# Kernel tuning notes

Measured on AMD Instinct MI355X. Metric: run time of the kernel, lower is better.

Reference implementation:

```python
import jax, jax.numpy as jnp
import numpy as np

N = 50000; FIN = 64; H = 128; E = 800000; T = 8
P = 250000; D = 500000; G = 20000; V = 2000; O = 2


def _mp(h, Ws, Wn, b, edge_src, edge_dst, n):
    # mean-aggregation message passing: relu(h Ws + mean_neigh(h) Wn + b)
    deg = jax.ops.segment_sum(jnp.ones(edge_dst.shape[0], h.dtype), edge_dst, n)
    agg = jax.ops.segment_sum(h[edge_src], edge_dst, n) / jnp.maximum(deg, 1.0)[:, None]
    return jax.nn.relu(h @ Ws + agg @ Wn + b)


def _forward(x, W_enc_self, W_enc_nei, b_enc, W2_self, W2_nei, b2, Wd1, bd1, Wd2, bd2,
             counts, edge_src, edge_dst, place_idx, src_idx, t_idx, dst_nodes, dst_seg,
             group_id, variant_of_group):
    n = x.shape[0]
    p = place_idx.shape[0]
    g = variant_of_group.shape[0]
    v = counts.shape[0]
    # first encoder, then T sequential second_encoder applications (feature generations)
    h0 = _mp(x, W_enc_self, W_enc_nei, b_enc, edge_src, edge_dst, n)

    def step(h, _):
        h2 = _mp(h, W2_self, W2_nei, b2, edge_src, edge_dst, n)
        return h2, h2

    _, hs = jax.lax.scan(step, h0, None, length=T)
    feats = jnp.concatenate([h0[None], hs], axis=0)  # [T+1, N, H]

    # gather (place, src) features at the generation index of each prediction
    place_f = feats[t_idx, place_idx]                 # [P, H]
    src_f = feats[t_idx, src_idx]                     # [P, H]
    # dst feature = sum over the destination set of each prediction
    dst_f = jax.ops.segment_sum(feats[t_idx[dst_seg], dst_nodes], dst_seg, p)  # [P, H]

    cat = jnp.concatenate([place_f, src_f, dst_f], axis=-1)  # [P, 3H]
    logits = jax.nn.relu(cat @ Wd1 + bd1) @ Wd2 + bd2        # [P, O]
    logprob = jax.nn.log_softmax(logits, axis=-1)            # [P, O]

    # prev_prob: inclusive running sum of per-step logprob sums within each variant
    group_sums = jax.ops.segment_sum(logprob, group_id, g)   # [G, O]
    cum = jnp.cumsum(group_sums, axis=0)
    var_tot = jax.ops.segment_sum(group_sums, variant_of_group, v)
    var_excl = jnp.cumsum(var_tot, axis=0) - var_tot
    within = cum - var_excl[variant_of_group]                # [G, O]
    prev = within[group_id]                                  # [P, O]

    logc = jnp.log(counts / jnp.sum(counts))                 # log(count/total) per variant
    add = logprob + prev + logc[variant_of_group[group_id]][:, None]
    return jnp.zeros((n, logits.shape[-1]), x.dtype).at[place_idx].add(add)


def setup_inputs() -> dict:
    ks = jax.random.split(jax.random.key(0), 24)
    s = jnp.float32(0.05)
    f32 = jnp.float32
    i32 = jnp.int32
    return {
        "x": jax.random.normal(ks[0], (N, FIN), f32),
        "W_enc_self": jax.random.normal(ks[1], (FIN, H), f32) * s,
        "W_enc_nei": jax.random.normal(ks[2], (FIN, H), f32) * s,
        "b_enc": jax.random.normal(ks[3], (H,), f32) * s,
        "W2_self": jax.random.normal(ks[4], (H, H), f32) * s,
        "W2_nei": jax.random.normal(ks[5], (H, H), f32) * s,
        "b2": jax.random.normal(ks[6], (H,), f32) * s,
        "Wd1": jax.random.normal(ks[7], (3 * H, 3 * H), f32) * s,
        "bd1": jax.random.normal(ks[8], (3 * H,), f32) * s,
        "Wd2": jax.random.normal(ks[9], (3 * H, O), f32) * s,
        "bd2": jax.random.normal(ks[10], (O,), f32) * s,
        "counts": jax.random.uniform(ks[11], (V,), f32) + 0.5,
        "edge_src": jax.random.randint(ks[12], (E,), 0, N, i32),
        "edge_dst": jax.random.randint(ks[13], (E,), 0, N, i32),
        "place_idx": jax.random.randint(ks[14], (P,), 0, N, i32),
        "src_idx": jax.random.randint(ks[15], (P,), 0, N, i32),
        "t_idx": jax.random.randint(ks[16], (P,), 0, T + 1, i32),
        "dst_nodes": jax.random.randint(ks[17], (D,), 0, N, i32),
        "dst_seg": jnp.sort(jax.random.randint(ks[18], (D,), 0, P, i32)),
        "group_id": jnp.sort(jax.random.randint(ks[19], (P,), 0, G, i32)),
        "variant_of_group": jnp.sort(jax.random.randint(ks[20], (G,), 0, V, i32)),
    }


def reference(x, W_enc_self, W_enc_nei, b_enc, W2_self, W2_nei, b2, Wd1, bd1, Wd2, bd2,
              counts, edge_src, edge_dst, place_idx, src_idx, t_idx, dst_nodes, dst_seg,
              group_id, variant_of_group):
    return _forward(x, W_enc_self, W_enc_nei, b_enc, W2_self, W2_nei, b2, Wd1, bd1, Wd2, bd2,
                    counts, edge_src, edge_dst, place_idx, src_idx, t_idx, dst_nodes, dst_seg,
                    group_id, variant_of_group)
```

## Files before the change

kernel.cpp:

```cpp
#include <hip/hip_runtime.h>
#include <math.h>

#define NN 50000
#define FINN 64
#define HD 128
#define EE 800000
#define TT 8
#define PP 250000
#define DD 500000
#define GG 20000
#define VV 2000
#define OO 2

typedef short short8 __attribute__((ext_vector_type(8)));
typedef float f32x4 __attribute__((ext_vector_type(4)));

__device__ __forceinline__ unsigned short f2bf(float f) {
    unsigned int u = __float_as_uint(f);
    u += 0x7fffu + ((u >> 16) & 1u);
    return (unsigned short)(u >> 16);
}
__device__ __forceinline__ float bf2f(unsigned short u) {
    return __uint_as_float(((unsigned int)u) << 16);
}

struct us8 { unsigned short v[8]; };

__device__ __forceinline__ void gload_lds16(const void* g, void* l) {
    __builtin_amdgcn_global_load_lds((__attribute__((address_space(1))) void*)g,
                                     (__attribute__((address_space(3))) void*)l, 16, 0, 0);
}

__global__ void count_k(const int* __restrict__ idx, int* __restrict__ counts, int n) {
    int i = blockIdx.x * blockDim.x + threadIdx.x;
    if (i < n) atomicAdd(&counts[idx[i]], 1);
}

__global__ void blk_sum_k(const int* __restrict__ counts, int n, int* __restrict__ bsum) {
    __shared__ int buf[256];
    int t = threadIdx.x, i = blockIdx.x * 256 + t;
    buf[t] = (i < n) ? counts[i] : 0;
    __syncthreads();
    for (int off = 128; off > 0; off >>= 1) {
        if (t < off) buf[t] += buf[t + off];
        __syncthreads();
    }
    if (t == 0) bsum[blockIdx.x] = buf[0];
}

__global__ void scan_small_k(const int* __restrict__ bsum, int nb, int* __restrict__ boff) {
    __shared__ int buf[256];
    int t = threadIdx.x;
    int v = (t < nb) ? bsum[t] : 0;
    buf[t] = v;
    __syncthreads();
    for (int off = 1; off < 256; off <<= 1) {
        int u = (t >= off) ? buf[t - off] : 0;
        __syncthreads();
        buf[t] += u;
        __syncthreads();
    }
    if (t < nb) boff[t] = buf[t] - v;
}

__global__ void rowptr_fill_k(const int* __restrict__ counts, const int* __restrict__ boff,
                              int n, int* __restrict__ rowptr, int total) {
    __shared__ int buf[256];
    int t = threadIdx.x, i = blockIdx.x * 256 + t;
    int v = (i < n) ? counts[i] : 0;
    buf[t] = v;
    __syncthreads();
    for (int off = 1; off < 256; off <<= 1) {
        int u = (t >= off) ? buf[t - off] : 0;
        __syncthreads();
        buf[t] += u;
        __syncthreads();
    }
    if (i < n) rowptr[i] = boff[blockIdx.x] + buf[t] - v;
    if (i == 0) rowptr[n] = total;
}

__global__ void lb_rowptr_k(const int* __restrict__ arr, int n, int* __restrict__ rowptr, int m) {
    int i = blockIdx.x * blockDim.x + threadIdx.x;
    if (i > m) return;
    int lo = 0, hi = n;
    while (lo < hi) {
        int mid = (lo + hi) >> 1;
        if (arr[mid] < i) lo = mid + 1; else hi = mid;
    }
    rowptr[i] = lo;
}

__global__ void fill_csr_k(const int* __restrict__ esrc, const int* __restrict__ edst,
                           const int* __restrict__ rowptr, int* __restrict__ cursor,
                           int* __restrict__ outi, int n) {
    int e = blockIdx.x * blockDim.x + threadIdx.x;
    if (e < n) {
        int d = edst[e];
        int pos = atomicAdd(&cursor[d], 1);
        outi[rowptr[d] + pos] = esrc[e];
    }
}

__global__ void hist9_k(const int* __restrict__ t_idx, int* __restrict__ hist) {
    __shared__ int l[9];
    if (threadIdx.x < 9) l[threadIdx.x] = 0;
    __syncthreads();
    int p = blockIdx.x * 256 + threadIdx.x;
    if (p < PP) atomicAdd(&l[t_idx[p]], 1);
    __syncthreads();
    if (threadIdx.x < 9) atomicAdd(&hist[threadIdx.x], l[threadIdx.x]);
}

__global__ void scan9_k(const int* __restrict__ hist, int* __restrict__ boff9) {
    if (threadIdx.x == 0) {
        int a = 0;
        for (int i = 0; i < 9; ++i) { boff9[i] = a; a += hist[i]; }
    }
}

__global__ void bucket_perm_k(const int* __restrict__ t_idx, const int* __restrict__ boff9,
                              int* __restrict__ cursor9, int* __restrict__ pperm) {
    __shared__ int lcnt[9];
    __shared__ int lbase[9];
    int tid = threadIdx.x;
    int p = blockIdx.x * 256 + tid;
    if (tid < 9) lcnt[tid] = 0;
    __syncthreads();
    int t = 0, lr = 0;
    bool ok = p < PP;
    if (ok) {
        t = t_idx[p];
        lr = atomicAdd(&lcnt[t], 1);
    }
    __syncthreads();
    if (tid < 9) lbase[tid] = atomicAdd(&cursor9[tid], lcnt[tid]);
    __syncthreads();
    if (ok) pperm[boff9[t] + lbase[t] + lr] = p;
}

__global__ void prep_k(const float* __restrict__ x,
                       const float* __restrict__ Wes, const float* __restrict__ Wen,
                       const float* __restrict__ W2s, const float* __restrict__ W2n,
                       const float* __restrict__ Wd1,
                       unsigned short* __restrict__ xb, unsigned short* __restrict__ wenc_t,
                       unsigned short* __restrict__ w2_t, unsigned short* __restrict__ wd1t) {
    int i = blockIdx.x * 256 + threadIdx.x;
    if (i < NN * FINN) xb[i] = f2bf(x[i]);
    if (i < HD * 2 * FINN) {
        int c = i / (2 * FINN), k = i - c * (2 * FINN);
        wenc_t[i] = f2bf((k < FINN) ? Wes[k * HD + c] : Wen[(k - FINN) * HD + c]);
    }
    if (i < HD * 2 * HD) {
        int c = i / (2 * HD), k = i - c * (2 * HD);
        w2_t[i] = f2bf((k < HD) ? W2s[k * HD + c] : W2n[(k - HD) * HD + c]);
    }
    if (i < 384 * 384) {
        int n = i / 384, k = i - n * 384;
        wd1t[i] = f2bf(Wd1[k * 384 + n]);
    }
}

template <int KIN>
__launch_bounds__(256)
__global__ void agg2_k(const unsigned short* __restrict__ h, const int* __restrict__ rowptr,
                       const int* __restrict__ csr_src, unsigned short* __restrict__ aggout) {
    constexpr int LPR = KIN >> 3;
    constexpr int EPW = 64 / LPR;
    int node = blockIdx.x * 4 + (threadIdx.x >> 6);
    int lane = threadIdx.x & 63;
    int sub = lane / LPR;
    int fl = lane % LPR;
    if (node >= NN) return;
    int s = rowptr[node], e = rowptr[node + 1];
    float acc[8] = {};
    int i = s + sub;
    int iB = i + EPW;
    int srcA = (i < e) ? csr_src[i] : 0;
    int srcB = (iB < e) ? csr_src[iB] : 0;
    while (i < e) {
        bool hB = iB < e;
        us8 vA = *(const us8*)&h[(size_t)srcA * KIN + fl * 8];
        us8 vB;
        if (hB) vB = *(const us8*)&h[(size_t)srcB * KIN + fl * 8];
        int iN = iB + EPW, iN2 = iN + EPW;
        srcA = (iN < e) ? csr_src[iN] : 0;
        srcB = (iN2 < e) ? csr_src[iN2] : 0;
#pragma unroll
        for (int j = 0; j < 8; ++j) acc[j] += bf2f(vA.v[j]);
        if (hB) {
#pragma unroll
            for (int j = 0; j < 8; ++j) acc[j] += bf2f(vB.v[j]);
        }
        i = iN; iB = iN2;
    }
#pragma unroll
    for (int m = LPR; m < 64; m <<= 1)
#pragma unroll
        for (int j = 0; j < 8; ++j) acc[j] += __shfl_xor(acc[j], m);
    if (sub == 0) {
        float d = fmaxf((float)(e - s), 1.f);
        us8 o;
#pragma unroll
        for (int j = 0; j < 8; ++j) o.v[j] = f2bf(acc[j] / d);
        *(us8*)&aggout[(size_t)node * KIN + fl * 8] = o;
    }
}

__launch_bounds__(128)
__global__ void mp_mfma_k(const unsigned short* __restrict__ hin,
                          const unsigned short* __restrict__ aggin,
                          const unsigned short* __restrict__ Wt,
                          const float* __restrict__ bias,
                          unsigned short* __restrict__ hout, int Kin) {
    int tid = threadIdx.x;
    int lane = tid & 63, w = tid >> 6;
    int cc = lane & 15, g = lane >> 4;
    int K = 2 * Kin;
    int rowA = blockIdx.x * 32 + w * 16 + cc;
    bool rowok = rowA < NN;
    const unsigned short* hrow = hin + (size_t)rowA * Kin;
    const unsigned short* arow = aggin + (size_t)rowA * Kin;

    f32x4 acc[8];
#pragma unroll
    for (int t = 0; t < 8; ++t) acc[t] = (f32x4){0.f, 0.f, 0.f, 0.f};

    for (int k0 = 0; k0 < K; k0 += 32) {
        int k = k0 + g * 8;
        short8 a = {0, 0, 0, 0, 0, 0, 0, 0};
        if (rowok)
            a = *(const short8*)((k < Kin) ? (hrow + k) : (arow + (k - Kin)));
#pragma unroll
        for (int t = 0; t < 8; ++t) {
            short8 b = *(const short8*)&Wt[(size_t)(t * 16 + cc) * K + k];
            acc[t] = __builtin_amdgcn_mfma_f32_16x16x32_bf16(a, b, acc[t], 0, 0, 0);
        }
    }
#pragma unroll
    for (int t = 0; t < 8; ++t) {
        int col = t * 16 + cc;
        float b1 = bias[col];
#pragma unroll
        for (int r = 0; r < 4; ++r) {
            int grow = blockIdx.x * 32 + w * 16 + g * 4 + r;
            if (grow < NN)
                hout[(size_t)grow * HD + col] = f2bf(fmaxf(acc[t][r] + b1, 0.f));
        }
    }
}

__launch_bounds__(256)
__global__ void dst_sum_k(const unsigned short* __restrict__ feats,
                          const int* __restrict__ t_idx, const int* __restrict__ dst_nodes,
                          const int* __restrict__ dst_rowptr, const int* __restrict__ pperm,
                          unsigned short* __restrict__ dstc) {
    int pi = blockIdx.x * 4 + (threadIdx.x >> 6);
    int lane = threadIdx.x & 63;
    int sub = lane >> 4;
    int fl = lane & 15;
    if (pi >= PP) return;
    int p = pperm[pi];
    long t = t_idx[p];
    const unsigned short* base = feats + t * (long)NN * HD;
    int s = dst_rowptr[p], e = dst_rowptr[p + 1];
    float acc[8] = {};
    int i = s + sub;
    int nd_next = (i < e) ? dst_nodes[i] : 0;
    for (; i < e; i += 4) {
        int nd = nd_next;
        int in = i + 4;
        if (in < e) nd_next = dst_nodes[in];
        us8 v = *(const us8*)&base[(size_t)nd * HD + fl * 8];
#pragma unroll
        for (int j = 0; j < 8; ++j) acc[j] += bf2f(v.v[j]);
    }
#pragma unroll
    for (int m = 16; m < 64; m <<= 1)
#pragma unroll
        for (int j = 0; j < 8; ++j) acc[j] += __shfl_xor(acc[j], m);
    if (sub == 0) {
        us8 o;
#pragma unroll
        for (int j = 0; j < 8; ++j) o.v[j] = f2bf(acc[j]);
        *(us8*)&dstc[(size_t)pi * HD + fl * 8] = o;
    }
}

__launch_bounds__(256)
__global__ void dec3_k(const unsigned short* __restrict__ feats,
                       const unsigned short* __restrict__ dstc,
                       const int* __restrict__ place_idx, const int* __restrict__ src_idx,
                       const int* __restrict__ t_idx, const int* __restrict__ group_id,
                       const int* __restrict__ pperm,
                       const unsigned short* __restrict__ Wd1t,
                       const float* __restrict__ bd1, const float* __restrict__ Wd2,
                       const float* __restrict__ bd2, float* __restrict__ logprob,
                       float* __restrict__ group_sums) {
    __shared__ unsigned short lds_a[192 * 128];
    __shared__ const unsigned short* rowbase[192];
    __shared__ float lpart[4][64][2];

    int tid = threadIdx.x;
    int lane = tid & 63, w = tid >> 6;
    int cc = lane & 15, gq = lane >> 4;
    int p0 = blockIdx.x * 64;

    if (tid < 192) {
        int sec = tid >> 6, pl = tid & 63;
        int pic = min(p0 + pl, PP - 1);
        const unsigned short* b;
        if (sec == 2) {
            b = dstc + (size_t)pic * HD;
        } else {
            int p = pperm[pic];
            long t = t_idx[p];
            int node = (sec == 0) ? place_idx[p] : src_idx[p];
            b = feats + ((t * NN + node) * (long)HD);
        }
        rowbase[tid] = b;
    }
    __syncthreads();

    {
        int chunk = lane & 15;
        int rsub = lane >> 4;
#pragma unroll
        for (int i = 0; i < 12; ++i) {
            int r = w * 48 + i * 4 + rsub;
            const unsigned short* src = rowbase[r] + ((chunk ^ (r & 7)) * 8);
            gload_lds16(src, &lds_a[(size_t)(w * 48 + i * 4) * 128]);
        }
    }
    __syncthreads();

    f32x4 acc[4][6];
#pragma unroll
    for (int s = 0; s < 4; ++s)
#pragma unroll
        for (int t = 0; t < 6; ++t) acc[s][t] = (f32x4){0.f, 0.f, 0.f, 0.f};

    const unsigned short* bbase = Wd1t + ((long)(w * 96 + cc) * 384 + gq * 8);
    int cx7 = cc & 7;

#pragma unroll
    for (int kk = 0; kk < 12; ++kk) {
        int sec = kk >> 2;
        int cbase = (kk & 3) * 4 + gq;
        int coff = (cbase ^ cx7) * 8;
        short8 a_c[4];
#pragma unroll
        for (int s = 0; s < 4; ++s) {
            int lrow = sec * 64 + s * 16 + cc;
            a_c[s] = *(const short8*)&lds_a[(size_t)lrow * 128 + coff];
        }
#pragma unroll
        for (int t = 0; t < 6; ++t) {
            short8 b = *(const short8*)(bbase + (long)t * 16 * 384 + kk * 32);
#pragma unroll
            for (int s = 0; s < 4; ++s)
                acc[s][t] = __builtin_amdgcn_mfma_f32_16x16x32_bf16(a_c[s], b, acc[s][t], 0, 0, 0);
        }
    }

    float part[4][4][2] = {};
#pragma unroll
    for (int t = 0; t < 6; ++t) {
        int col = w * 96 + t * 16 + cc;
        float b1 = bd1[col];
        float w0 = Wd2[col * 2 + 0], w1 = Wd2[col * 2 + 1];
#pragma unroll
        for (int s = 0; s < 4; ++s)
#pragma unroll
            for (int r = 0; r < 4; ++r) {
                float h = fmaxf(acc[s][t][r] + b1, 0.f);
                part[s][r][0] += h * w0;
                part[s][r][1] += h * w1;
            }
    }
#pragma unroll
    for (int m = 1; m < 16; m <<= 1)
#pragma unroll
        for (int s = 0; s < 4; ++s)
#pragma unroll
            for (int r = 0; r < 4; ++r) {
                part[s][r][0] += __shfl_xor(part[s][r][0], m);
                part[s][r][1] += __shfl_xor(part[s][r][1], m);
            }
    if (cc == 0) {
#pragma unroll
        for (int s = 0; s < 4; ++s)
#pragma unroll
            for (int r = 0; r < 4; ++r) {
                int row = s * 16 + gq * 4 + r;
                lpart[w][row][0] = part[s][r][0];
                lpart[w][row][1] = part[s][r][1];
            }
    }
    __syncthreads();
    if (tid < 64) {
        int pi = p0 + tid;
        if (pi < PP) {
            int p = pperm[pi];
            float l0 = lpart[0][tid][0] + lpart[1][tid][0] + lpart[2][tid][0] + lpart[3][tid][0] + bd2[0];
            float l1 = lpart[0][tid][1] + lpart[1][tid][1] + lpart[2][tid][1] + lpart[3][tid][1] + bd2[1];
            float m = fmaxf(l0, l1);
            float lse = m + logf(expf(l0 - m) + expf(l1 - m));
            float lp0 = l0 - lse, lp1 = l1 - lse;
            logprob[p * 2 + 0] = lp0;
            logprob[p * 2 + 1] = lp1;
            int g = group_id[p];
            atomicAdd(&group_sums[g * 2 + 0], lp0);
            atomicAdd(&group_sums[g * 2 + 1], lp1);
        }
    }
}

__global__ void within_total_k(const float* __restrict__ group_sums,
                               const int* __restrict__ var_rowptr,
                               const float* __restrict__ counts,
                               float* __restrict__ within, float* __restrict__ total) {
    __shared__ float buf[256];
    int tid = threadIdx.x;
    float s = 0.f;
    for (int i = tid; i < VV; i += 256) s += counts[i];
    buf[tid] = s;
    __syncthreads();
    for (int off = 128; off > 0; off >>= 1) {
        if (tid < off) buf[tid] += buf[tid + off];
        __syncthreads();
    }
    if (tid == 0) total[0] = buf[0];
    for (int v = tid; v < VV; v += 256) {
        int gs = var_rowptr[v], ge = var_rowptr[v + 1];
        float r0 = 0.f, r1 = 0.f;
        for (int g = gs; g < ge; ++g) {
            r0 += group_sums[2 * g + 0];
            r1 += group_sums[2 * g + 1];
            within[2 * g + 0] = r0;
            within[2 * g + 1] = r1;
        }
    }
}

__global__ void final_k(const float* __restrict__ logprob, const float* __restrict__ within,
                        const int* __restrict__ group_id, const int* __restrict__ vog,
                        const float* __restrict__ counts, const float* __restrict__ total,
                        const int* __restrict__ place_idx, float* __restrict__ outp) {
    int p = blockIdx.x * blockDim.x + threadIdx.x;
    if (p >= PP) return;
    int g = group_id[p];
    int v = vog[g];
    float lc = logf(counts[v]) - logf(total[0]);
    int node = place_idx[p];
    atomicAdd(&outp[node * 2 + 0], logprob[p * 2 + 0] + within[g * 2 + 0] + lc);
    atomicAdd(&outp[node * 2 + 1], logprob[p * 2 + 1] + within[g * 2 + 1] + lc);
}

extern "C" void kernel_launch(void* const* d_in, const int* in_sizes, int n_in,
                              void* d_out, int out_size, void* d_ws, size_t ws_size,
                              hipStream_t stream) {
    const float* x          = (const float*)d_in[0];
    const float* W_enc_self = (const float*)d_in[1];
    const float* W_enc_nei  = (const float*)d_in[2];
    const float* b_enc      = (const float*)d_in[3];
    const float* W2_self    = (const float*)d_in[4];
    const float* W2_nei     = (const float*)d_in[5];
    const float* b2         = (const float*)d_in[6];
    const float* Wd1        = (const float*)d_in[7];
    const float* bd1        = (const float*)d_in[8];
    const float* Wd2        = (const float*)d_in[9];
    const float* bd2        = (const float*)d_in[10];
    const float* counts     = (const float*)d_in[11];
    const int* edge_src     = (const int*)d_in[12];
    const int* edge_dst     = (const int*)d_in[13];
    const int* place_idx    = (const int*)d_in[14];
    const int* src_idx      = (const int*)d_in[15];
    const int* t_idx        = (const int*)d_in[16];
    const int* dst_nodes    = (const int*)d_in[17];
    const int* dst_seg      = (const int*)d_in[18];
    const int* group_id     = (const int*)d_in[19];
    const int* variant_of_group = (const int*)d_in[20];
    float* outp = (float*)d_out;

    const int NB = (NN + 255) / 256;

    unsigned short* feats = (unsigned short*)d_ws;
    unsigned short* aggb  = feats + (size_t)(TT + 1) * NN * HD;
    unsigned short* xb    = aggb + (size_t)NN * HD;
    unsigned short* dstc  = xb + (size_t)NN * FINN;
    unsigned short* wenc_t = dstc + (size_t)PP * HD;
    unsigned short* w2_t   = wenc_t + HD * 2 * FINN;
    unsigned short* wd1t   = w2_t + HD * 2 * HD;
    int* zr = (int*)(wd1t + 384 * 384);
    int* csr_counts   = zr;
    int* csr_cursor   = csr_counts + NN;
    float* group_sums = (float*)(csr_cursor + NN);
    int* hist9        = (int*)(group_sums + 2 * GG);
    int* cursor9      = hist9 + 9;
    size_t zero_words = (size_t)NN + NN + 2 * GG + 18;
    int* bsum       = cursor9 + 9;
    int* boff       = bsum + 256;
    int* boff9      = boff + 256;
    int* csr_rowptr = boff9 + 16;
    int* dst_rowptr = csr_rowptr + (NN + 1);
    int* var_rowptr = dst_rowptr + (PP + 1);
    int* csr_src    = var_rowptr + (VV + 1);
    int* pperm      = csr_src + EE;
    float* logprob  = (float*)(pperm + PP);
    float* within   = logprob + 2 * PP;
    float* total_counts = within + 2 * GG;

    hipMemsetAsync(zr, 0, zero_words * 4, stream);
    hipMemsetAsync(d_out, 0, (size_t)out_size * sizeof(float), stream);

    prep_k<<<(NN * FINN + 255) / 256, 256, 0, stream>>>(x, W_enc_self, W_enc_nei, W2_self,
                                                        W2_nei, Wd1, xb, wenc_t, w2_t, wd1t);
    count_k<<<(EE + 255) / 256, 256, 0, stream>>>(edge_dst, csr_counts, EE);
    blk_sum_k<<<NB, 256, 0, stream>>>(csr_counts, NN, bsum);
    scan_small_k<<<1, 256, 0, stream>>>(bsum, NB, boff);
    rowptr_fill_k<<<NB, 256, 0, stream>>>(csr_counts, boff, NN, csr_rowptr, EE);
    fill_csr_k<<<(EE + 255) / 256, 256, 0, stream>>>(edge_src, edge_dst, csr_rowptr,
                                                     csr_cursor, csr_src, EE);
    lb_rowptr_k<<<(PP + 256) / 256, 256, 0, stream>>>(dst_seg, DD, dst_rowptr, PP);
    lb_rowptr_k<<<(VV + 256) / 256, 256, 0, stream>>>(variant_of_group, GG, var_rowptr, VV);
    hist9_k<<<(PP + 255) / 256, 256, 0, stream>>>(t_idx, hist9);
    scan9_k<<<1, 64, 0, stream>>>(hist9, boff9);
    bucket_perm_k<<<(PP + 255) / 256, 256, 0, stream>>>(t_idx, boff9, cursor9, pperm);

    for (int r = 0; r <= TT; ++r) {
        const unsigned short* hin = (r == 0) ? xb : feats + (size_t)(r - 1) * NN * HD;
        unsigned short* hout = feats + (size_t)r * NN * HD;
        if (r == 0) {
            agg2_k<FINN><<<(NN + 3) / 4, 256, 0, stream>>>(hin, csr_rowptr, csr_src, aggb);
            mp_mfma_k<<<(NN + 31) / 32, 128, 0, stream>>>(hin, aggb, wenc_t, b_enc, hout, FINN);
        } else {
            agg2_k<HD><<<(NN + 3) / 4, 256, 0, stream>>>(hin, csr_rowptr, csr_src, aggb);
            mp_mfma_k<<<(NN + 31) / 32, 128, 0, stream>>>(hin, aggb, w2_t, b2, hout, HD);
        }
    }

    dst_sum_k<<<(PP + 3) / 4, 256, 0, stream>>>(feats, t_idx, dst_nodes, dst_rowptr, pperm, dstc);
    dec3_k<<<(PP + 63) / 64, 256, 0, stream>>>(feats, dstc, place_idx, src_idx, t_idx,
                                               group_id, pperm, wd1t, bd1, Wd2, bd2,
                                               logprob, group_sums);

    within_total_k<<<1, 256, 0, stream>>>(group_sums, var_rowptr, counts, within, total_counts);
    final_k<<<(PP + 255) / 256, 256, 0, stream>>>(logprob, within, group_id, variant_of_group,
                                                  counts, total_counts, place_idx, outp);
}
```

Measured before the change: 1.132 ms.

## Make decoder kernel persistent with double-buffered LDS gathers and register-resident weights

The decoder kernel becomes persistent: a fixed grid of 256 blocks loops over the row tiles. Each block keeps its whole Wd1 slice in registers instead of reloading it for every tile. Row gathers into LDS are double-buffered and their index and pointer lookups are prefetched several tiles ahead, so global-to-LDS loads overlap the MFMA work of the previous tile. The cost is heavy register pressure (72 short8 values per thread, launch bounds of 1) and hand-written waitcnt and barrier handling that could be fragile.

```diff
diff --git a/kernel.cpp b/kernel.cpp
--- a/kernel.cpp
+++ b/kernel.cpp
@@ -11,6 +11,9 @@
 #define GG 20000
 #define VV 2000
 #define OO 2
+
+#define DEC_GRID 256
+#define DEC_TILES ((PP + 63) / 64)
 
 typedef short short8 __attribute__((ext_vector_type(8)));
 typedef float f32x4 __attribute__((ext_vector_type(4)));
@@ -287,8 +290,8 @@
     }
 }
 
-__launch_bounds__(256)
-__global__ void dec3_k(const unsigned short* __restrict__ feats,
+__launch_bounds__(256, 1)
+__global__ void dec4_k(const unsigned short* __restrict__ feats,
                        const unsigned short* __restrict__ dstc,
                        const int* __restrict__ place_idx, const int* __restrict__ src_idx,
                        const int* __restrict__ t_idx, const int* __restrict__ group_id,
@@ -297,123 +300,170 @@
                        const float* __restrict__ bd1, const float* __restrict__ Wd2,
                        const float* __restrict__ bd2, float* __restrict__ logprob,
                        float* __restrict__ group_sums) {
-    __shared__ unsigned short lds_a[192 * 128];
-    __shared__ const unsigned short* rowbase[192];
+    __shared__ unsigned short buf[2][192 * 128];
+    __shared__ unsigned long long rb[2][192];
     __shared__ float lpart[4][64][2];
 
     int tid = threadIdx.x;
     int lane = tid & 63, w = tid >> 6;
     int cc = lane & 15, gq = lane >> 4;
-    int p0 = blockIdx.x * 64;
-
+    int cx7 = cc & 7;
+    int bid = blockIdx.x;
+
+    int row = min(tid, 191);
+    int sec = row >> 6, pl = row & 63;
+    const int* nptr = (sec == 0) ? place_idx : src_idx;
+
+    int nt = (DEC_TILES - 1 - bid) / DEC_GRID + 1;
+
+    int pic0 = min(bid * 64 + pl, PP - 1);
+    int pic1 = min((bid + DEC_GRID) * 64 + pl, PP - 1);
+    int pic2p = min((bid + 2 * DEC_GRID) * 64 + pl, PP - 1);
+    int pA = pperm[pic0], pB = pperm[pic1];
+    int preg = pperm[pic2p];
+    int tA = t_idx[pA], tB = t_idx[pB];
+    int nA = nptr[pA], nB = nptr[pB];
     if (tid < 192) {
-        int sec = tid >> 6, pl = tid & 63;
-        int pic = min(p0 + pl, PP - 1);
-        const unsigned short* b;
-        if (sec == 2) {
-            b = dstc + (size_t)pic * HD;
-        } else {
-            int p = pperm[pic];
-            long t = t_idx[p];
-            int node = (sec == 0) ? place_idx[p] : src_idx[p];
-            b = feats + ((t * NN + node) * (long)HD);
-        }
-        rowbase[tid] = b;
-    }
-    __syncthreads();
-
+        rb[0][tid] = (sec == 2) ? (unsigned long long)(dstc + (size_t)pic0 * HD)
+                                : (unsigned long long)(feats + (((long)tA * NN + nA) * (long)HD));
+        rb[1][tid] = (sec == 2) ? (unsigned long long)(dstc + (size_t)pic1 * HD)
+                                : (unsigned long long)(feats + (((long)tB * NN + nB) * (long)HD));
+    }
+
+    short8 breg[72];
     {
-        int chunk = lane & 15;
-        int rsub = lane >> 4;
-#pragma unroll
-        for (int i = 0; i < 12; ++i) {
-            int r = w * 48 + i * 4 + rsub;
-            const unsigned short* src = rowbase[r] + ((chunk ^ (r & 7)) * 8);
-            gload_lds16(src, &lds_a[(size_t)(w * 48 + i * 4) * 128]);
-        }
-    }
-    __syncthreads();
-
-    f32x4 acc[4][6];
-#pragma unroll
-    for (int s = 0; s < 4; ++s)
-#pragma unroll
-        for (int t = 0; t < 6; ++t) acc[s][t] = (f32x4){0.f, 0.f, 0.f, 0.f};
-
-    const unsigned short* bbase = Wd1t + ((long)(w * 96 + cc) * 384 + gq * 8);
-    int cx7 = cc & 7;
-
-#pragma unroll
-    for (int kk = 0; kk < 12; ++kk) {
-        int sec = kk >> 2;
-        int cbase = (kk & 3) * 4 + gq;
-        int coff = (cbase ^ cx7) * 8;
-        short8 a_c[4];
-#pragma unroll
-        for (int s = 0; s < 4; ++s) {
-            int lrow = sec * 64 + s * 16 + cc;
-            a_c[s] = *(const short8*)&lds_a[(size_t)lrow * 128 + coff];
-        }
+        const unsigned short* bbase = Wd1t + ((long)(w * 96 + cc) * 384 + gq * 8);
+#pragma unroll
+        for (int kk = 0; kk < 12; ++kk)
+#pragma unroll
+            for (int t = 0; t < 6; ++t)
+                breg[kk * 6 + t] = *(const short8*)(bbase + (long)t * 16 * 384 + kk * 32);
+    }
+    __syncthreads();
+
+    int rsub = lane >> 4, chunk = lane & 15;
+
+#define STAGE(par_)                                                                  \
+    {                                                                                \
+        _Pragma("unroll")                                                            \
+        for (int i = 0; i < 12; ++i) {                                               \
+            int r = w * 48 + i * 4 + rsub;                                           \
+            const unsigned short* src =                                              \
+                (const unsigned short*)rb[par_][r] + ((chunk ^ (r & 7)) * 8);        \
+            gload_lds16(src, &buf[par_][(w * 48 + i * 4) * 128]);                    \
+        }                                                                            \
+    }
+
+    STAGE(0);
+
+    for (int k = 0; k < nt; ++k) {
+        int par = k & 1, npar = par ^ 1;
+        int tl = bid + k * DEC_GRID;
+
+        int tload = t_idx[preg];
+        int nload = nptr[preg];
+        int pic3v = min((bid + (k + 3) * DEC_GRID) * 64 + pl, PP - 1);
+        int preg2 = pperm[pic3v];
+        int pic2v = min((bid + (k + 2) * DEC_GRID) * 64 + pl, PP - 1);
+
+        STAGE(npar);
+
+        __builtin_amdgcn_sched_barrier(0);
+        asm volatile("s_waitcnt vmcnt(15)" ::: "memory");
+        __builtin_amdgcn_s_barrier();
+        __builtin_amdgcn_sched_barrier(0);
+
+        const unsigned short* bufc = &buf[par][0];
+        f32x4 acc[4][6];
+#pragma unroll
+        for (int s = 0; s < 4; ++s)
+#pragma unroll
+            for (int t = 0; t < 6; ++t) acc[s][t] = (f32x4){0.f, 0.f, 0.f, 0.f};
+
+#pragma unroll
+        for (int kk = 0; kk < 12; ++kk) {
+            int seck = kk >> 2;
+            int cbase = (kk & 3) * 4 + gq;
+            int coff = (cbase ^ cx7) * 8;
+            short8 a_c[4];
+#pragma unroll
+            for (int s = 0; s < 4; ++s) {
+                int lrow = seck * 64 + s * 16 + cc;
+                a_c[s] = *(const short8*)&bufc[lrow * 128 + coff];
+            }
+#pragma unroll
+            for (int t = 0; t < 6; ++t)
+#pragma unroll
+                for (int s = 0; s < 4; ++s)
+                    acc[s][t] = __builtin_amdgcn_mfma_f32_16x16x32_bf16(a_c[s], breg[kk * 6 + t],
+                                                                        acc[s][t], 0, 0, 0);
+        }
+
+        float part[4][4][2] = {};
 #pragma unroll
         for (int t = 0; t < 6; ++t) {
-            short8 b = *(const short8*)(bbase + (long)t * 16 * 384 + kk * 32);
+            int col = w * 96 + t * 16 + cc;
+            float b1 = bd1[col];
+            float w0 = Wd2[col * 2 + 0], w1 = Wd2[col * 2 + 1];
 #pragma unroll
             for (int s = 0; s < 4; ++s)
-                acc[s][t] = __builtin_amdgcn_mfma_f32_16x16x32_bf16(a_c[s], b, acc[s][t], 0, 0, 0);
-        }
-    }
-
-    float part[4][4][2] = {};
-#pragma unroll
-    for (int t = 0; t < 6; ++t) {
-        int col = w * 96 + t * 16 + cc;
-        float b1 = bd1[col];
-        float w0 = Wd2[col * 2 + 0], w1 = Wd2[col * 2 + 1];
-#pragma unroll
-        for (int s = 0; s < 4; ++s)
-#pragma unroll
-            for (int r = 0; r < 4; ++r) {
-                float h = fmaxf(acc[s][t][r] + b1, 0.f);
-                part[s][r][0] += h * w0;
-                part[s][r][1] += h * w1;
+#pragma unroll
+                for (int r = 0; r < 4; ++r) {
+                    float h = fmaxf(acc[s][t][r] + b1, 0.f);
+                    part[s][r][0] += h * w0;
+                    part[s][r][1] += h * w1;
+                }
+        }
+#pragma unroll
+        for (int m = 1; m < 16; m <<= 1)
+#pragma unroll
+            for (int s = 0; s < 4; ++s)
+#pragma unroll
+                for (int r = 0; r < 4; ++r) {
+                    part[s][r][0] += __shfl_xor(part[s][r][0], m);
+                    part[s][r][1] += __shfl_xor(part[s][r][1], m);
+                }
+        if (cc == 0) {
+#pragma unroll
+            for (int s = 0; s < 4; ++s)
+#pragma unroll
+                for (int r = 0; r < 4; ++r) {
+                    int orow = s * 16 + gq * 4 + r;
+                    lpart[w][orow][0] = part[s][r][0];
+                    lpart[w][orow][1] = part[s][r][1];
+                }
+        }
+
+        if (tid < 192)
+            rb[par][tid] = (sec == 2)
+                               ? (unsigned long long)(dstc + (size_t)pic2v * HD)
+                               : (unsigned long long)(feats + (((long)tload * NN + nload) * (long)HD));
+        preg = preg2;
+
+        asm volatile("s_waitcnt lgkmcnt(0)" ::: "memory");
+        __builtin_amdgcn_s_barrier();
+        __builtin_amdgcn_sched_barrier(0);
+
+        if (tid < 64) {
+            int pi = tl * 64 + tid;
+            if (pi < PP) {
+                int p = pperm[pi];
+                float l0 = lpart[0][tid][0] + lpart[1][tid][0] + lpart[2][tid][0] +
+                           lpart[3][tid][0] + bd2[0];
+                float l1 = lpart[0][tid][1] + lpart[1][tid][1] + lpart[2][tid][1] +
+                           lpart[3][tid][1] + bd2[1];
+                float m = fmaxf(l0, l1);
+                float lse = m + logf(expf(l0 - m) + expf(l1 - m));
+                float lp0 = l0 - lse, lp1 = l1 - lse;
+                logprob[p * 2 + 0] = lp0;
+                logprob[p * 2 + 1] = lp1;
+                int g = group_id[p];
+                atomicAdd(&group_sums[g * 2 + 0], lp0);
+                atomicAdd(&group_sums[g * 2 + 1], lp1);
             }
-    }
-#pragma unroll
-    for (int m = 1; m < 16; m <<= 1)
-#pragma unroll
-        for (int s = 0; s < 4; ++s)
-#pragma unroll
-            for (int r = 0; r < 4; ++r) {
-                part[s][r][0] += __shfl_xor(part[s][r][0], m);
-                part[s][r][1] += __shfl_xor(part[s][r][1], m);
-            }
-    if (cc == 0) {
-#pragma unroll
-        for (int s = 0; s < 4; ++s)
-#pragma unroll
-            for (int r = 0; r < 4; ++r) {
-                int row = s * 16 + gq * 4 + r;
-                lpart[w][row][0] = part[s][r][0];
-                lpart[w][row][1] = part[s][r][1];
-            }
-    }
-    __syncthreads();
-    if (tid < 64) {
-        int pi = p0 + tid;
-        if (pi < PP) {
-            int p = pperm[pi];
-            float l0 = lpart[0][tid][0] + lpart[1][tid][0] + lpart[2][tid][0] + lpart[3][tid][0] + bd2[0];
-            float l1 = lpart[0][tid][1] + lpart[1][tid][1] + lpart[2][tid][1] + lpart[3][tid][1] + bd2[1];
-            float m = fmaxf(l0, l1);
-            float lse = m + logf(expf(l0 - m) + expf(l1 - m));
-            float lp0 = l0 - lse, lp1 = l1 - lse;
-            logprob[p * 2 + 0] = lp0;
-            logprob[p * 2 + 1] = lp1;
-            int g = group_id[p];
-            atomicAdd(&group_sums[g * 2 + 0], lp0);
-            atomicAdd(&group_sums[g * 2 + 1], lp1);
-        }
-    }
+        }
+    }
+#undef STAGE
 }
 
 __global__ void within_total_k(const float* __restrict__ group_sums,
@@ -541,9 +591,9 @@
     }
 
     dst_sum_k<<<(PP + 3) / 4, 256, 0, stream>>>(feats, t_idx, dst_nodes, dst_rowptr, pperm, dstc);
-    dec3_k<<<(PP + 63) / 64, 256, 0, stream>>>(feats, dstc, place_idx, src_idx, t_idx,
-                                               group_id, pperm, wd1t, bd1, Wd2, bd2,
-                                               logprob, group_sums);
+    dec4_k<<<DEC_GRID, 256, 0, stream>>>(feats, dstc, place_idx, src_idx, t_idx,
+                                         group_id, pperm, wd1t, bd1, Wd2, bd2,
+                                         logprob, group_sums);
 
     within_total_k<<<1, 256, 0, stream>>>(group_sums, var_rowptr, counts, within, total_counts);
     final_k<<<(PP + 255) / 256, 256, 0, stream>>>(logprob, within, group_id, variant_of_group,
```

Measured after the change: 1.084 ms. -4.2%, faster.
